# Kernel tuning notes

Hardware: AMD Instinct MI355X
Metric: run time of the kernel (lower is better)

Reference implementation:

```python
import jax, jax.numpy as jnp
import numpy as np
import math

EPS_NORM = 1e-6
EPS_COS = 1e-6
B, L, LC = 2, 2048, 1024
D_MODEL, D_CROSS, D_HEAD = 1024, 1024, 64
N_HEADS = D_MODEL // D_HEAD


def setup_inputs() -> dict:
    key = jax.random.key(0)
    ks = jax.random.split(key, 6)
    x = jax.random.normal(ks[0], (B, L, D_MODEL), jnp.float32)
    pos = jax.random.uniform(ks[1], (B, L, 2), dtype=jnp.float32)  # normalized 2D canvas coords
    x_cross = jax.random.normal(ks[2], (B, LC, D_CROSS), jnp.float32)
    norm_scale = jnp.ones((D_MODEL,), jnp.float32)          # RMSNorm scale (init ones)
    norm_cross_scale = jnp.ones((D_CROSS,), jnp.float32)
    q_w = jax.random.normal(ks[3], (D_MODEL, D_MODEL), jnp.float32) / math.sqrt(D_MODEL)
    kv_w = jax.random.normal(ks[4], (D_CROSS, 2 * D_MODEL), jnp.float32) / math.sqrt(D_CROSS)
    # out_proj is zero-init in the original; use small random weights so the block is non-trivial
    out_w = jax.random.normal(ks[5], (D_MODEL, D_MODEL), jnp.float32) / math.sqrt(D_MODEL)
    scale = jnp.full((N_HEADS,), 10.0, jnp.float32)          # learned per-head cosine-sim scale
    # AxialRoPE2D freqs (k-diffusion style, learnable_freqs=False): [n_heads, d_head//4]
    log_min, log_max = math.log(math.pi), math.log(10.0 * math.pi)
    freqs = jnp.exp(jnp.linspace(log_min, log_max, N_HEADS * D_HEAD // 4 + 1)[:-1])
    freqs = freqs.reshape(D_HEAD // 4, N_HEADS).T            # [H, E//4]
    return dict(x=x, pos=pos, x_cross=x_cross, norm_scale=norm_scale,
                norm_cross_scale=norm_cross_scale, q_w=q_w, kv_w=kv_w,
                scale=scale, out_w=out_w, freqs=freqs)


def _rms_norm(x, scale, eps=EPS_NORM):
    ms = jnp.mean(jnp.square(x), axis=-1, keepdims=True)
    return x * (scale * jax.lax.rsqrt(ms + eps))


def reference(x, pos, x_cross, norm_scale, norm_cross_scale, q_w, kv_w, scale, out_w, freqs):
    skip = x
    xn = _rms_norm(x, norm_scale)
    xc = _rms_norm(x_cross, norm_cross_scale)
    q = xn @ q_w                                             # [B,L,D]
    kv = xc @ kv_w                                           # [B,LC,2D]
    q = q.reshape(B, L, N_HEADS, D_HEAD).transpose(0, 2, 1, 3)      # [B,H,L,E]
    kv = kv.reshape(B, LC, 2, N_HEADS, D_HEAD)               # split (t nh e), t outermost
    k = kv[:, :, 0].transpose(0, 2, 1, 3)                    # [B,H,LC,E]
    v = kv[:, :, 1].transpose(0, 2, 1, 3)
    # per-head cosine-sim QK scaling
    sq = jnp.sqrt(scale)[:, None, None]                      # [H,1,1]
    q = q * (sq * jax.lax.rsqrt(jnp.sum(jnp.square(q), -1, keepdims=True) + EPS_COS))
    k = k * (sq * jax.lax.rsqrt(jnp.sum(jnp.square(k), -1, keepdims=True) + EPS_COS))
    # axial 2D RoPE on q only (as in the original forward)
    theta = jnp.concatenate([pos[..., None, 0:1] * freqs,
                             pos[..., None, 1:2] * freqs], -1)      # [B,L,H,E//2]
    theta = jnp.moveaxis(theta, -2, -3)                      # [B,H,L,E//2]
    d = theta.shape[-1]
    q1, q2 = q[..., :d], q[..., d:]
    cos, sin = jnp.cos(theta), jnp.sin(theta)
    q = jnp.concatenate([q1 * cos - q2 * sin, q2 * cos + q1 * sin], -1)
    # SDPA with scale=1.0 (cosine-sim scaling already applied)
    attn = jax.nn.softmax(jnp.einsum('bhqe,bhke->bhqk', q, k), axis=-1)
    o = jnp.einsum('bhqk,bhke->bhqe', attn, v)
    o = o.transpose(0, 2, 1, 3).reshape(B, L, D_MODEL)       # merge heads
    return o @ out_w + skip
```

## Files before the change

kernel.cpp:

```cpp
#include <hip/hip_runtime.h>
#include <math.h>

typedef unsigned short u16;
typedef __bf16 bf16x8 __attribute__((ext_vector_type(8)));
typedef float f32x4 __attribute__((ext_vector_type(4)));

#define EPS_NORM 1e-6f
#define EPS_COS  1e-6f

static constexpr int Bc = 2;
static constexpr int Lq = 2048;
static constexpr int Lc = 1024;
static constexpr int Dm = 1024;
static constexpr int DH = 64;
static constexpr int NH = 16;

#define F32MODE(probe) ((probe)[0] == 0x3F800000u)

__device__ __forceinline__ float b2f(u16 u) {
  union { unsigned u; float f; } x; x.u = ((unsigned)u) << 16; return x.f;
}
__device__ __forceinline__ u16 f2b(float f) {
  union { float f; unsigned u; } x; x.f = f;
  unsigned v = x.u;
  v += 0x7fffu + ((v >> 16) & 1u);
  return (u16)(v >> 16);
}
__device__ __forceinline__ unsigned pkbf(float lo, float hi) {
#if __has_builtin(__builtin_amdgcn_cvt_pk_bf16_f32)
  return __builtin_bit_cast(unsigned, __builtin_amdgcn_cvt_pk_bf16_f32(lo, hi));
#else
  return (unsigned)f2b(lo) | ((unsigned)f2b(hi) << 16);
#endif
}
__device__ __forceinline__ float loadf(const void* p, size_t i, bool f32m) {
  return f32m ? ((const float*)p)[i] : b2f(((const u16*)p)[i]);
}
__device__ __forceinline__ void gll16(const u16* g, u16* l) {
  __builtin_amdgcn_global_load_lds(
      (const __attribute__((address_space(1))) unsigned*)g,
      (__attribute__((address_space(3))) unsigned*)l, 16, 0, 0);
}

__global__ __launch_bounds__(256) void transpose3_kernel(
    const void* __restrict__ qw, const void* __restrict__ kvw,
    const void* __restrict__ outw, u16* __restrict__ wqw,
    u16* __restrict__ wkvw, u16* __restrict__ woutw,
    const unsigned* __restrict__ probe) {
  bool f32m = F32MODE(probe);
  __shared__ u16 tile[32][33];
  int id = blockIdx.x;
  const void* src; u16* dst; int N;
  if (id < 1024)      { src = qw;   dst = wqw;   N = Dm; }
  else if (id < 3072) { src = kvw;  dst = wkvw;  N = 2 * Dm; id -= 1024; }
  else                { src = outw; dst = woutw; N = Dm;     id -= 3072; }
  int k0 = (id & 31) * 32, n0 = (id >> 5) * 32;
  int tn = threadIdx.x & 31, tg = threadIdx.x >> 5;
#pragma unroll
  for (int r = 0; r < 4; r++) {
    int k = tg * 4 + r;
    tile[k][tn] = f2b(loadf(src, (size_t)(k0 + k) * N + n0 + tn, f32m));
  }
  __syncthreads();
#pragma unroll
  for (int r = 0; r < 4; r++) {
    int n = tg * 4 + r;
    dst[(size_t)(n0 + n) * Dm + k0 + tn] = tile[tn][n];
  }
}

__global__ __launch_bounds__(128) void rmsnorm2_kernel(
    const void* __restrict__ x, const void* __restrict__ xcr,
    const void* __restrict__ nsc, const void* __restrict__ ncs,
    u16* __restrict__ xn, u16* __restrict__ xc,
    const unsigned* __restrict__ probe) {
  bool f32m = F32MODE(probe);
  int row = blockIdx.x;
  const void* src; const void* sc; u16* dst;
  if (row < Bc * Lq) { src = x; sc = nsc; dst = xn; }
  else { row -= Bc * Lq; src = xcr; sc = ncs; dst = xc; }
  int t = threadIdx.x;
  float f[8]; float ss = 0.f;
  if (f32m) {
    const float* xr = (const float*)src + (size_t)row * Dm + t * 8;
    float4 a = *(const float4*)(xr), b = *(const float4*)(xr + 4);
    f[0]=a.x; f[1]=a.y; f[2]=a.z; f[3]=a.w; f[4]=b.x; f[5]=b.y; f[6]=b.z; f[7]=b.w;
  } else {
    union { uint4 u4; u16 s[8]; } v;
    v.u4 = *(const uint4*)((const u16*)src + (size_t)row * Dm + t * 8);
#pragma unroll
    for (int i = 0; i < 8; i++) f[i] = b2f(v.s[i]);
  }
#pragma unroll
  for (int i = 0; i < 8; i++) ss += f[i] * f[i];
#pragma unroll
  for (int o = 32; o > 0; o >>= 1) ss += __shfl_xor(ss, o, 64);
  __shared__ float red[2];
  if ((t & 63) == 0) red[t >> 6] = ss;
  __syncthreads();
  float inv = rsqrtf((red[0] + red[1]) / (float)Dm + EPS_NORM);
  union { uint4 u4; u16 s[8]; } ov;
#pragma unroll
  for (int i = 0; i < 8; i++) ov.s[i] = f2b(f[i] * loadf(sc, t * 8 + i, f32m) * inv);
  *(uint4*)(dst + (size_t)row * Dm + t * 8) = ov.u4;
}

__device__ __forceinline__ void gemm_body(
    const u16* __restrict__ A, const u16* __restrict__ Bt,
    int M, int N, int m0, int n0, int mode,
    u16* __restrict__ outb, u16* __restrict__ kfp, u16* __restrict__ vt,
    const void* __restrict__ skip, void* __restrict__ Cn,
    const void* __restrict__ scale, const void* __restrict__ pos,
    const void* __restrict__ freqs, bool f32m,
    u16 (&As)[2][4096], u16 (&Bs)[2][4096]) {
  constexpr int K = Dm;
  int t = threadIdx.x;
  int wv = t >> 6, lane = t & 63;
  int wr = wv >> 1, wc = wv & 1;
  int r16 = lane & 15, quad = lane >> 4;

  int i0 = t, i1 = 256 + t;
  int row0 = i0 >> 2, row1 = i1 >> 2;
  int gc0 = ((i0 & 3) - ((row0 >> 1) & 3)) & 3;
  int gc1 = ((i1 & 3) - ((row1 >> 1) & 3)) & 3;
  const u16* pA0 = A  + (size_t)(m0 + row0) * K + gc0 * 8;
  const u16* pA1 = A  + (size_t)(m0 + row1) * K + gc1 * 8;
  const u16* pB0 = Bt + (size_t)(n0 + row0) * K + gc0 * 8;
  const u16* pB1 = Bt + (size_t)(n0 + row1) * K + gc1 * 8;
  int iA0 = (wv * 64) * 8, iA1 = (256 + wv * 64) * 8;

  int spos = (quad + ((r16 >> 1) & 3)) & 3;
  int offA[4], offB[4];
#pragma unroll
  for (int i = 0; i < 4; i++) {
    offA[i] = ((wr * 64 + i * 16 + r16) * 4 + spos) * 8;
    offB[i] = ((wc * 64 + i * 16 + r16) * 4 + spos) * 8;
  }

  f32x4 acc[4][4] = {};

  gll16(pA0, &As[0][iA0]); gll16(pA1, &As[0][iA1]);
  gll16(pB0, &Bs[0][iA0]); gll16(pB1, &Bs[0][iA1]);

  int niter = K >> 5;
  for (int it = 0; it < niter; ++it) {
    __syncthreads();
    if (it + 1 < niter) {
      int koff = (it + 1) << 5;
      int nb = (it + 1) & 1;
      gll16(pA0 + koff, &As[nb][iA0]); gll16(pA1 + koff, &As[nb][iA1]);
      gll16(pB0 + koff, &Bs[nb][iA0]); gll16(pB1 + koff, &Bs[nb][iA1]);
    }
    const u16* Ab = As[it & 1];
    const u16* Bb = Bs[it & 1];
    bf16x8 af[4], bf[4];
#pragma unroll
    for (int i = 0; i < 4; i++) {
      af[i] = __builtin_bit_cast(bf16x8, *(const uint4*)(Ab + offA[i]));
      bf[i] = __builtin_bit_cast(bf16x8, *(const uint4*)(Bb + offB[i]));
    }
#pragma unroll
    for (int mt = 0; mt < 4; mt++)
#pragma unroll
      for (int nt = 0; nt < 4; nt++)
        acc[mt][nt] = __builtin_amdgcn_mfma_f32_16x16x32_bf16(
            af[mt], bf[nt], acc[mt][nt], 0, 0, 0);
  }

  if (mode == 2) {
#pragma unroll
    for (int mt = 0; mt < 4; mt++)
#pragma unroll
      for (int nt = 0; nt < 4; nt++)
#pragma unroll
        for (int r = 0; r < 4; r++) {
          int m = m0 + wr * 64 + mt * 16 + quad * 4 + r;
          int n = n0 + wc * 64 + nt * 16 + r16;
          size_t idx = (size_t)m * N + n;
          float v = acc[mt][nt][r] + loadf(skip, idx, f32m);
          if (f32m) ((float*)Cn)[idx] = v;
          else      outb[idx] = f2b(v);
        }
    return;
  }

  int col0 = n0 + wc * 64;
  if (mode == 1 && col0 >= Dm) {
    int hh = (col0 - Dm) >> 6;
#pragma unroll
    for (int mt = 0; mt < 4; mt++)
#pragma unroll
      for (int r = 0; r < 4; r++) {
        int m = m0 + wr * 64 + mt * 16 + quad * 4 + r;
        int bb = m >> 10, lc = m & (Lc - 1);
        u16* tb = vt + ((size_t)(bb * NH + hh) * 16 + (lc >> 6)) * 4096;
        int kin = lc & 63;
#pragma unroll
        for (int nt = 0; nt < 4; nt++) {
          int d = nt * 16 + r16;
          tb[d * 64 + ((kin >> 3) ^ (d & 7)) * 8 + (kin & 7)] = f2b(acc[mt][nt][r]);
        }
      }
    return;
  }

  int hh = (col0 & (Dm - 1)) >> 6;
  float sqs = sqrtf(loadf(scale, hh, f32m));
  float fr = (mode == 0) ? loadf(freqs, hh * 16 + r16, f32m) : 0.f;
#pragma unroll
  for (int mt = 0; mt < 4; mt++) {
    float ss[4];
#pragma unroll
    for (int r = 0; r < 4; r++) {
      ss[r] = 0.f;
#pragma unroll
      for (int nt = 0; nt < 4; nt++) ss[r] += acc[mt][nt][r] * acc[mt][nt][r];
    }
#pragma unroll
    for (int o = 1; o < 16; o <<= 1)
#pragma unroll
      for (int r = 0; r < 4; r++) ss[r] += __shfl_xor(ss[r], o, 64);
#pragma unroll
    for (int r = 0; r < 4; r++) {
      int m = m0 + wr * 64 + mt * 16 + quad * 4 + r;
      float inv = sqs * rsqrtf(ss[r] + EPS_COS);
      if (mode == 1) {
        int bb = m >> 10, lc = m & (Lc - 1);
        size_t base = ((size_t)((bb * NH + hh) * Lc) + lc) * 64;
#pragma unroll
        for (int nt = 0; nt < 4; nt++)
          kfp[base + nt * 16 + r16] = f2b(acc[mt][nt][r] * inv);
      } else {
        int bb = m >> 11, l = m & (Lq - 1);
        float p0 = loadf(pos, (size_t)m * 2 + 0, f32m);
        float p1 = loadf(pos, (size_t)m * 2 + 1, f32m);
        size_t base = ((size_t)((bb * NH + hh) * Lq) + l) * 64;
#pragma unroll
        for (int nt = 0; nt < 2; nt++) {
          float th = (nt ? p1 : p0) * fr;
          float c, s;
          sincosf(th, &s, &c);
          float lo = acc[mt][nt][r] * inv, hi = acc[mt][nt + 2][r] * inv;
          outb[base + nt * 16 + r16]       = f2b(lo * c - hi * s);
          outb[base + (nt + 2) * 16 + r16] = f2b(hi * c + lo * s);
        }
      }
    }
  }
}

__global__ __launch_bounds__(256) void qkv_gemm_kernel(
    const u16* __restrict__ xn, const u16* __restrict__ wqw,
    const u16* __restrict__ xc, const u16* __restrict__ wkvw,
    u16* __restrict__ qf, u16* __restrict__ kf, u16* __restrict__ vt,
    const void* __restrict__ scale, const void* __restrict__ pos,
    const void* __restrict__ freqs, const unsigned* __restrict__ probe) {
  __shared__ u16 As[2][4096];
  __shared__ u16 Bs[2][4096];
  bool f32m = F32MODE(probe);
  int blk = blockIdx.x;
  if (blk < 256) {
    gemm_body(xn, wqw, Bc * Lq, Dm, (blk >> 3) * 128, (blk & 7) * 128, 0,
              qf, nullptr, nullptr, nullptr, nullptr, scale, pos, freqs,
              f32m, As, Bs);
  } else {
    int id = blk - 256;
    gemm_body(xc, wkvw, Bc * Lc, 2 * Dm, (id >> 4) * 128, (id & 15) * 128, 1,
              nullptr, kf, vt, nullptr, nullptr, scale, nullptr, nullptr,
              f32m, As, Bs);
  }
}

__global__ __launch_bounds__(256) void final_gemm_kernel(
    const u16* __restrict__ ob, const u16* __restrict__ woutw,
    const void* __restrict__ skip, void* __restrict__ Cn,
    u16* __restrict__ outb, const unsigned* __restrict__ probe) {
  __shared__ u16 As[2][4096];
  __shared__ u16 Bs[2][4096];
  bool f32m = F32MODE(probe);
  int blk = blockIdx.x;
  gemm_body(ob, woutw, Bc * Lq, Dm, (blk >> 3) * 128, (blk & 7) * 128, 2,
            outb, nullptr, nullptr, skip, Cn, nullptr, nullptr, nullptr,
            f32m, As, Bs);
}

__global__ __launch_bounds__(256) void attn_kernel(
    const u16* __restrict__ qf, const u16* __restrict__ kf,
    const u16* __restrict__ vt, u16* __restrict__ o_out,
    const void* __restrict__ scale, const unsigned* __restrict__ probe) {
  __shared__ u16 Kt[2][4096];
  __shared__ u16 Vs[2][4096];
  __shared__ u16 Pl[4][2][1024];

  int blk = blockIdx.x;
  int bh = blk & 31;
  int qt = blk >> 5;
  int h = bh & 15;
  bool f32m = F32MODE(probe);
  float sh = loadf(scale, h, f32m);
  const u16* kbase = kf + (size_t)bh * Lc * DH;
  const u16* vtb   = vt + (size_t)bh * 16 * 4096;
  int t = threadIdx.x;
  int wv = t >> 6, lane = t & 63;
  int r16 = lane & 15, quad = lane >> 4;

  const u16* qb0 = qf + ((size_t)bh * Lq + qt * 128 + wv * 16) * DH;
  const u16* qb1 = qb0 + 64 * DH;
  bf16x8 af00 = __builtin_bit_cast(bf16x8, *(const uint4*)(qb0 + r16 * DH + 0  + quad * 8));
  bf16x8 af01 = __builtin_bit_cast(bf16x8, *(const uint4*)(qb0 + r16 * DH + 32 + quad * 8));
  bf16x8 af10 = __builtin_bit_cast(bf16x8, *(const uint4*)(qb1 + r16 * DH + 0  + quad * 8));
  bf16x8 af11 = __builtin_bit_cast(bf16x8, *(const uint4*)(qb1 + r16 * DH + 32 + quad * 8));

  int e0 = t, e1 = 256 + t;
  int row0 = e0 >> 3, g0 = (e0 & 7) ^ (row0 & 7);
  int row1 = e1 >> 3, g1 = (e1 & 7) ^ (row1 & 7);
  const u16* pK0 = kbase + (size_t)row0 * DH + g0 * 8;
  const u16* pK1 = kbase + (size_t)row1 * DH + g1 * 8;
  const u16* pV0 = vtb + e0 * 8;
  const u16* pV1 = vtb + e1 * 8;
  int iS0 = (wv * 64) * 8, iS1 = (256 + wv * 64) * 8;
  int kphys0 = ((quad)     ^ (r16 & 7)) * 8;
  int kphys1 = ((4 | quad) ^ (r16 & 7)) * 8;

  float l0[4] = {0.f, 0.f, 0.f, 0.f}, l1[4] = {0.f, 0.f, 0.f, 0.f};
  f32x4 oa0[4] = {{0,0,0,0},{0,0,0,0},{0,0,0,0},{0,0,0,0}};
  f32x4 oa1[4] = {{0,0,0,0},{0,0,0,0},{0,0,0,0},{0,0,0,0}};

  gll16(pK0, &Kt[0][iS0]); gll16(pK1, &Kt[0][iS1]);
  gll16(pV0, &Vs[0][iS0]); gll16(pV1, &Vs[0][iS1]);

  for (int it = 0; it < Lc / 64; ++it) {
    __syncthreads();
    if (it + 1 < Lc / 64) {
      size_t koff = (size_t)(it + 1) * 64 * DH;
      size_t voff = (size_t)(it + 1) * 4096;
      int nb = (it + 1) & 1;
      gll16(pK0 + koff, &Kt[nb][iS0]);
      gll16(pK1 + koff, &Kt[nb][iS1]);
      gll16(pV0 + voff, &Vs[nb][iS0]);
      gll16(pV1 + voff, &Vs[nb][iS1]);
    }
    const u16* Kb = Kt[it & 1];
    const u16* Vb = Vs[it & 1];

    f32x4 s0[4], s1[4];
#pragma unroll
    for (int nt = 0; nt < 4; nt++) {
      int nrow = (nt * 16 + r16) * 64;
      bf16x8 bf0 = __builtin_bit_cast(bf16x8, *(const uint4*)(Kb + nrow + kphys0));
      bf16x8 bf1 = __builtin_bit_cast(bf16x8, *(const uint4*)(Kb + nrow + kphys1));
      s0[nt] = (f32x4){0.f, 0.f, 0.f, 0.f};
      s0[nt] = __builtin_amdgcn_mfma_f32_16x16x32_bf16(af00, bf0, s0[nt], 0, 0, 0);
      s0[nt] = __builtin_amdgcn_mfma_f32_16x16x32_bf16(af01, bf1, s0[nt], 0, 0, 0);
      s1[nt] = (f32x4){0.f, 0.f, 0.f, 0.f};
      s1[nt] = __builtin_amdgcn_mfma_f32_16x16x32_bf16(af10, bf0, s1[nt], 0, 0, 0);
      s1[nt] = __builtin_amdgcn_mfma_f32_16x16x32_bf16(af11, bf1, s1[nt], 0, 0, 0);
    }

#pragma unroll
    for (int set = 0; set < 2; set++) {
      u16* P = &Pl[wv][set][0];
#pragma unroll
      for (int r = 0; r < 4; r++) {
        f32x4* s = set ? s1 : s0;
        float p0 = __expf(s[0][r] - sh);
        float p1 = __expf(s[1][r] - sh);
        float p2 = __expf(s[2][r] - sh);
        float p3 = __expf(s[3][r] - sh);
        if (set) l1[r] += (p0 + p1) + (p2 + p3);
        else     l0[r] += (p0 + p1) + (p2 + p3);
        unsigned pa = pkbf(p0, p1), pb = pkbf(p2, p3);
        int mrow = quad * 4 + r;
        int bx = mrow & 7;
        int base = mrow * 64 + (r16 & 7);
        int c0 = (r16 >> 3);
        P[base + ((c0    ) ^ bx) * 8] = (u16)pa;
        P[base + ((c0 + 2) ^ bx) * 8] = (u16)(pa >> 16);
        P[base + ((c0 + 4) ^ bx) * 8] = (u16)pb;
        P[base + ((c0 + 6) ^ bx) * 8] = (u16)(pb >> 16);
      }
    }

#pragma unroll
    for (int dt = 0; dt < 4; dt++) {
      int vrow = (dt * 16 + r16) * 64;
#pragma unroll
      for (int kc = 0; kc < 2; kc++) {
        int ph = kc ? kphys1 : kphys0;
        bf16x8 bu  = __builtin_bit_cast(bf16x8, *(const uint4*)(Vb + vrow + ph));
        bf16x8 au0 = __builtin_bit_cast(bf16x8, *(const uint4*)&Pl[wv][0][r16 * 64 + ph]);
        bf16x8 au1 = __builtin_bit_cast(bf16x8, *(const uint4*)&Pl[wv][1][r16 * 64 + ph]);
        oa0[dt] = __builtin_amdgcn_mfma_f32_16x16x32_bf16(au0, bu, oa0[dt], 0, 0, 0);
        oa1[dt] = __builtin_amdgcn_mfma_f32_16x16x32_bf16(au1, bu, oa1[dt], 0, 0, 0);
      }
    }
  }

  int b = bh >> 4;
#pragma unroll
  for (int set = 0; set < 2; set++) {
    float* lr = set ? l1 : l0;
    f32x4* oa = set ? oa1 : oa0;
    float inv[4];
#pragma unroll
    for (int r = 0; r < 4; r++) {
      float l = lr[r];
#pragma unroll
      for (int o = 8; o > 0; o >>= 1) l += __shfl_xor(l, o, 64);
      inv[r] = 1.f / l;
    }
#pragma unroll
    for (int dt = 0; dt < 4; dt++)
#pragma unroll
      for (int r = 0; r < 4; r++) {
        int m = qt * 128 + set * 64 + wv * 16 + quad * 4 + r;
        o_out[((size_t)(b * Lq + m)) * Dm + h * DH + dt * 16 + r16] =
            f2b(oa[dt][r] * inv[r]);
      }
  }
}

extern "C" void kernel_launch(void* const* d_in, const int* in_sizes, int n_in,
                              void* d_out, int out_size, void* d_ws, size_t ws_size,
                              hipStream_t stream) {
  const void* x     = d_in[0];
  const void* pos   = d_in[1];
  const void* xcr   = d_in[2];
  const void* nsc   = d_in[3];
  const void* ncs   = d_in[4];
  const void* qw    = d_in[5];
  const void* kvw   = d_in[6];
  const void* scale = d_in[7];
  const void* outw  = d_in[8];
  const void* freqs = d_in[9];
  const unsigned* probe = (const unsigned*)nsc;

  char* ws = (char*)d_ws;
  const size_t MB = 1u << 20;
  u16*   wqw  = (u16*)(ws + 0 * MB);
  u16*   wkvw = (u16*)(ws + 2 * MB);
  u16*   woutw= (u16*)(ws + 6 * MB);
  u16*   xn   = (u16*)(ws + 8 * MB);
  u16*   ob   = (u16*)(ws + 8 * MB);
  u16*   xc   = (u16*)(ws + 16 * MB);
  u16*   qf   = (u16*)(ws + 20 * MB);
  u16*   kf   = (u16*)(ws + 28 * MB);
  u16*   vt   = (u16*)(ws + 32 * MB);

  transpose3_kernel<<<4096, 256, 0, stream>>>(qw, kvw, outw, wqw, wkvw, woutw, probe);
  rmsnorm2_kernel<<<Bc * Lq + Bc * Lc, 128, 0, stream>>>(x, xcr, nsc, ncs, xn, xc, probe);
  qkv_gemm_kernel<<<512, 256, 0, stream>>>(xn, wqw, xc, wkvw, qf, kf, vt,
                                           scale, pos, freqs, probe);
  attn_kernel<<<512, 256, 0, stream>>>(qf, kf, vt, ob, scale, probe);
  final_gemm_kernel<<<256, 256, 0, stream>>>(ob, woutw, x, d_out, (u16*)d_out, probe);
}
```

Measured before the change: 222.7 us.

## Double GEMM K-tile to 64 with XOR swizzle and fuse prep kernels

The shared GEMM body now stages 64-wide K slices instead of 32, using an XOR-swizzled LDS layout. This halves the number of barrier-separated iterations and doubles the MFMA work between syncs. The weight-transpose and RMSNorm kernels are merged into one launch, with RMSNorm moved to 256-thread blocks, to remove a launch and let both jobs run together. LDS use per GEMM block doubles to 64KB, which may reduce occupancy.

Result: no change. 222.3 us (-0.2%).

```diff
diff --git a/kernel.cpp b/kernel.cpp
--- a/kernel.cpp
+++ b/kernel.cpp
@@ -42,67 +42,65 @@
       (__attribute__((address_space(3))) unsigned*)l, 16, 0, 0);
 }
 
-__global__ __launch_bounds__(256) void transpose3_kernel(
+__global__ __launch_bounds__(256) void prep_kernel(
     const void* __restrict__ qw, const void* __restrict__ kvw,
     const void* __restrict__ outw, u16* __restrict__ wqw,
     u16* __restrict__ wkvw, u16* __restrict__ woutw,
-    const unsigned* __restrict__ probe) {
-  bool f32m = F32MODE(probe);
-  __shared__ u16 tile[32][33];
-  int id = blockIdx.x;
-  const void* src; u16* dst; int N;
-  if (id < 1024)      { src = qw;   dst = wqw;   N = Dm; }
-  else if (id < 3072) { src = kvw;  dst = wkvw;  N = 2 * Dm; id -= 1024; }
-  else                { src = outw; dst = woutw; N = Dm;     id -= 3072; }
-  int k0 = (id & 31) * 32, n0 = (id >> 5) * 32;
-  int tn = threadIdx.x & 31, tg = threadIdx.x >> 5;
-#pragma unroll
-  for (int r = 0; r < 4; r++) {
-    int k = tg * 4 + r;
-    tile[k][tn] = f2b(loadf(src, (size_t)(k0 + k) * N + n0 + tn, f32m));
-  }
-  __syncthreads();
-#pragma unroll
-  for (int r = 0; r < 4; r++) {
-    int n = tg * 4 + r;
-    dst[(size_t)(n0 + n) * Dm + k0 + tn] = tile[tn][n];
-  }
-}
-
-__global__ __launch_bounds__(128) void rmsnorm2_kernel(
     const void* __restrict__ x, const void* __restrict__ xcr,
     const void* __restrict__ nsc, const void* __restrict__ ncs,
     u16* __restrict__ xn, u16* __restrict__ xc,
     const unsigned* __restrict__ probe) {
   bool f32m = F32MODE(probe);
-  int row = blockIdx.x;
-  const void* src; const void* sc; u16* dst;
-  if (row < Bc * Lq) { src = x; sc = nsc; dst = xn; }
-  else { row -= Bc * Lq; src = xcr; sc = ncs; dst = xc; }
+  int id = blockIdx.x;
   int t = threadIdx.x;
-  float f[8]; float ss = 0.f;
-  if (f32m) {
-    const float* xr = (const float*)src + (size_t)row * Dm + t * 8;
-    float4 a = *(const float4*)(xr), b = *(const float4*)(xr + 4);
-    f[0]=a.x; f[1]=a.y; f[2]=a.z; f[3]=a.w; f[4]=b.x; f[5]=b.y; f[6]=b.z; f[7]=b.w;
+  if (id < 6144) {
+    int row = id;
+    const void* src; const void* sc; u16* dst;
+    if (row < Bc * Lq) { src = x; sc = nsc; dst = xn; }
+    else { row -= Bc * Lq; src = xcr; sc = ncs; dst = xc; }
+    float f[4]; float ss = 0.f;
+    if (f32m) {
+      float4 a = *(const float4*)((const float*)src + (size_t)row * Dm + t * 4);
+      f[0] = a.x; f[1] = a.y; f[2] = a.z; f[3] = a.w;
+    } else {
+      union { uint2 u2; u16 s[4]; } v;
+      v.u2 = *(const uint2*)((const u16*)src + (size_t)row * Dm + t * 4);
+#pragma unroll
+      for (int i = 0; i < 4; i++) f[i] = b2f(v.s[i]);
+    }
+#pragma unroll
+    for (int i = 0; i < 4; i++) ss += f[i] * f[i];
+#pragma unroll
+    for (int o = 32; o > 0; o >>= 1) ss += __shfl_xor(ss, o, 64);
+    __shared__ float red[4];
+    if ((t & 63) == 0) red[t >> 6] = ss;
+    __syncthreads();
+    float inv = rsqrtf((red[0] + red[1] + red[2] + red[3]) / (float)Dm + EPS_NORM);
+    union { uint2 u2; u16 s[4]; } ov;
+#pragma unroll
+    for (int i = 0; i < 4; i++) ov.s[i] = f2b(f[i] * loadf(sc, t * 4 + i, f32m) * inv);
+    *(uint2*)(dst + (size_t)row * Dm + t * 4) = ov.u2;
   } else {
-    union { uint4 u4; u16 s[8]; } v;
-    v.u4 = *(const uint4*)((const u16*)src + (size_t)row * Dm + t * 8);
-#pragma unroll
-    for (int i = 0; i < 8; i++) f[i] = b2f(v.s[i]);
-  }
-#pragma unroll
-  for (int i = 0; i < 8; i++) ss += f[i] * f[i];
-#pragma unroll
-  for (int o = 32; o > 0; o >>= 1) ss += __shfl_xor(ss, o, 64);
-  __shared__ float red[2];
-  if ((t & 63) == 0) red[t >> 6] = ss;
-  __syncthreads();
-  float inv = rsqrtf((red[0] + red[1]) / (float)Dm + EPS_NORM);
-  union { uint4 u4; u16 s[8]; } ov;
-#pragma unroll
-  for (int i = 0; i < 8; i++) ov.s[i] = f2b(f[i] * loadf(sc, t * 8 + i, f32m) * inv);
-  *(uint4*)(dst + (size_t)row * Dm + t * 8) = ov.u4;
+    id -= 6144;
+    __shared__ u16 tile[32][33];
+    const void* src; u16* dst; int N;
+    if (id < 1024)      { src = qw;   dst = wqw;   N = Dm; }
+    else if (id < 3072) { src = kvw;  dst = wkvw;  N = 2 * Dm; id -= 1024; }
+    else                { src = outw; dst = woutw; N = Dm;     id -= 3072; }
+    int k0 = (id & 31) * 32, n0 = (id >> 5) * 32;
+    int tn = t & 31, tg = t >> 5;
+#pragma unroll
+    for (int r = 0; r < 4; r++) {
+      int k = tg * 4 + r;
+      tile[k][tn] = f2b(loadf(src, (size_t)(k0 + k) * N + n0 + tn, f32m));
+    }
+    __syncthreads();
+#pragma unroll
+    for (int r = 0; r < 4; r++) {
+      int n = tg * 4 + r;
+      dst[(size_t)(n0 + n) * Dm + k0 + tn] = tile[tn][n];
+    }
+  }
 }
 
 __device__ __forceinline__ void gemm_body(
@@ -112,59 +110,69 @@
     const void* __restrict__ skip, void* __restrict__ Cn,
     const void* __restrict__ scale, const void* __restrict__ pos,
     const void* __restrict__ freqs, bool f32m,
-    u16 (&As)[2][4096], u16 (&Bs)[2][4096]) {
+    u16 (&As)[2][8192], u16 (&Bs)[2][8192]) {
   constexpr int K = Dm;
   int t = threadIdx.x;
   int wv = t >> 6, lane = t & 63;
   int wr = wv >> 1, wc = wv & 1;
   int r16 = lane & 15, quad = lane >> 4;
 
-  int i0 = t, i1 = 256 + t;
-  int row0 = i0 >> 2, row1 = i1 >> 2;
-  int gc0 = ((i0 & 3) - ((row0 >> 1) & 3)) & 3;
-  int gc1 = ((i1 & 3) - ((row1 >> 1) & 3)) & 3;
-  const u16* pA0 = A  + (size_t)(m0 + row0) * K + gc0 * 8;
-  const u16* pA1 = A  + (size_t)(m0 + row1) * K + gc1 * 8;
-  const u16* pB0 = Bt + (size_t)(n0 + row0) * K + gc0 * 8;
-  const u16* pB1 = Bt + (size_t)(n0 + row1) * K + gc1 * 8;
-  int iA0 = (wv * 64) * 8, iA1 = (256 + wv * 64) * 8;
-
-  int spos = (quad + ((r16 >> 1) & 3)) & 3;
-  int offA[4], offB[4];
-#pragma unroll
-  for (int i = 0; i < 4; i++) {
-    offA[i] = ((wr * 64 + i * 16 + r16) * 4 + spos) * 8;
-    offB[i] = ((wc * 64 + i * 16 + r16) * 4 + spos) * 8;
+  const u16* pA[4]; const u16* pB[4]; int iL[4];
+#pragma unroll
+  for (int c = 0; c < 4; c++) {
+    int i = c * 256 + t;
+    int row = i >> 3, g = (i & 7) ^ (row & 7);
+    pA[c] = A  + (size_t)(m0 + row) * K + g * 8;
+    pB[c] = Bt + (size_t)(n0 + row) * K + g * 8;
+    iL[c] = (c * 256 + wv * 64) * 8;
+  }
+
+  int offA[2][4], offB[2][4];
+#pragma unroll
+  for (int kh = 0; kh < 2; kh++) {
+    int pa = ((kh * 4 + quad) ^ (r16 & 7)) * 8;
+#pragma unroll
+    for (int i = 0; i < 4; i++) {
+      offA[kh][i] = (wr * 64 + i * 16 + r16) * 64 + pa;
+      offB[kh][i] = (wc * 64 + i * 16 + r16) * 64 + pa;
+    }
   }
 
   f32x4 acc[4][4] = {};
 
-  gll16(pA0, &As[0][iA0]); gll16(pA1, &As[0][iA1]);
-  gll16(pB0, &Bs[0][iA0]); gll16(pB1, &Bs[0][iA1]);
-
-  int niter = K >> 5;
+#pragma unroll
+  for (int c = 0; c < 4; c++) gll16(pA[c], &As[0][iL[c]]);
+#pragma unroll
+  for (int c = 0; c < 4; c++) gll16(pB[c], &Bs[0][iL[c]]);
+
+  int niter = K >> 6;
   for (int it = 0; it < niter; ++it) {
     __syncthreads();
     if (it + 1 < niter) {
-      int koff = (it + 1) << 5;
+      int koff = (it + 1) << 6;
       int nb = (it + 1) & 1;
-      gll16(pA0 + koff, &As[nb][iA0]); gll16(pA1 + koff, &As[nb][iA1]);
-      gll16(pB0 + koff, &Bs[nb][iA0]); gll16(pB1 + koff, &Bs[nb][iA1]);
+#pragma unroll
+      for (int c = 0; c < 4; c++) gll16(pA[c] + koff, &As[nb][iL[c]]);
+#pragma unroll
+      for (int c = 0; c < 4; c++) gll16(pB[c] + koff, &Bs[nb][iL[c]]);
     }
     const u16* Ab = As[it & 1];
     const u16* Bb = Bs[it & 1];
-    bf16x8 af[4], bf[4];
-#pragma unroll
-    for (int i = 0; i < 4; i++) {
-      af[i] = __builtin_bit_cast(bf16x8, *(const uint4*)(Ab + offA[i]));
-      bf[i] = __builtin_bit_cast(bf16x8, *(const uint4*)(Bb + offB[i]));
-    }
-#pragma unroll
-    for (int mt = 0; mt < 4; mt++)
-#pragma unroll
-      for (int nt = 0; nt < 4; nt++)
-        acc[mt][nt] = __builtin_amdgcn_mfma_f32_16x16x32_bf16(
-            af[mt], bf[nt], acc[mt][nt], 0, 0, 0);
+#pragma unroll
+    for (int kh = 0; kh < 2; kh++) {
+      bf16x8 af[4], bf[4];
+#pragma unroll
+      for (int i = 0; i < 4; i++) {
+        af[i] = __builtin_bit_cast(bf16x8, *(const uint4*)(Ab + offA[kh][i]));
+        bf[i] = __builtin_bit_cast(bf16x8, *(const uint4*)(Bb + offB[kh][i]));
+      }
+#pragma unroll
+      for (int mt = 0; mt < 4; mt++)
+#pragma unroll
+        for (int nt = 0; nt < 4; nt++)
+          acc[mt][nt] = __builtin_amdgcn_mfma_f32_16x16x32_bf16(
+              af[mt], bf[nt], acc[mt][nt], 0, 0, 0);
+    }
   }
 
   if (mode == 2) {
@@ -255,8 +263,8 @@
     u16* __restrict__ qf, u16* __restrict__ kf, u16* __restrict__ vt,
     const void* __restrict__ scale, const void* __restrict__ pos,
     const void* __restrict__ freqs, const unsigned* __restrict__ probe) {
-  __shared__ u16 As[2][4096];
-  __shared__ u16 Bs[2][4096];
+  __shared__ u16 As[2][8192];
+  __shared__ u16 Bs[2][8192];
   bool f32m = F32MODE(probe);
   int blk = blockIdx.x;
   if (blk < 256) {
@@ -275,8 +283,8 @@
     const u16* __restrict__ ob, const u16* __restrict__ woutw,
     const void* __restrict__ skip, void* __restrict__ Cn,
     u16* __restrict__ outb, const unsigned* __restrict__ probe) {
-  __shared__ u16 As[2][4096];
-  __shared__ u16 Bs[2][4096];
+  __shared__ u16 As[2][8192];
+  __shared__ u16 Bs[2][8192];
   bool f32m = F32MODE(probe);
   int blk = blockIdx.x;
   gemm_body(ob, woutw, Bc * Lq, Dm, (blk >> 3) * 128, (blk & 7) * 128, 2,
@@ -447,8 +455,8 @@
   u16*   kf   = (u16*)(ws + 28 * MB);
   u16*   vt   = (u16*)(ws + 32 * MB);
 
-  transpose3_kernel<<<4096, 256, 0, stream>>>(qw, kvw, outw, wqw, wkvw, woutw, probe);
-  rmsnorm2_kernel<<<Bc * Lq + Bc * Lc, 128, 0, stream>>>(x, xcr, nsc, ncs, xn, xc, probe);
+  prep_kernel<<<6144 + 4096, 256, 0, stream>>>(
+      qw, kvw, outw, wqw, wkvw, woutw, x, xcr, nsc, ncs, xn, xc, probe);
   qkv_gemm_kernel<<<512, 256, 0, stream>>>(xn, wqw, xc, wkvw, qf, kf, vt,
                                            scale, pos, freqs, probe);
   attn_kernel<<<512, 256, 0, stream>>>(qf, kf, vt, ob, scale, probe);
```
